# Kernel optimization log

Hardware: AMD Instinct MI355X
Metric: run time of the kernel (lower is better)

Reference implementation:

```python
import jax, jax.numpy as jnp
import numpy as np

B, L, HID = 32, 1, 3072
H, KV, D = 16, 8, 256
S = 2048
SCALE = D ** -0.5


def setup_inputs() -> dict:
    key = jax.random.key(0)
    ks = jax.random.split(key, 10)
    return {
        "hidden_states": jax.random.normal(ks[0], (B, L, HID), jnp.float32),
        "freqs_cos": jax.random.normal(ks[1], (B, L, D // 2), jnp.float32),
        "freqs_sin": jax.random.normal(ks[2], (B, L, D // 2), jnp.float32),
        "mask": jnp.zeros((B, 1, 1, S), jnp.float32),
        "cache_k": jax.random.normal(ks[3], (B, KV, S, D), jnp.float32),
        "cache_v": jax.random.normal(ks[4], (B, KV, S, D), jnp.float32),
        "wq": jax.random.normal(ks[5], (HID, H * D), jnp.float32) * 0.02,
        "wk": jax.random.normal(ks[6], (HID, KV * D), jnp.float32) * 0.02,
        "wv": jax.random.normal(ks[7], (HID, KV * D), jnp.float32) * 0.02,
        "wo": jax.random.normal(ks[8], (H * D, HID), jnp.float32) * 0.02,
        "pos": 2047,
    }


def _rope(x, cos, sin):
    # x: [B, L, nh, D]; cos/sin: [B, L, D/2]. Split-half complex rotation:
    # pairs are (x[..., i], x[..., i + D/2]), matching torch chunk+view_as_complex.
    half = x.shape[-1] // 2
    xr, xi = x[..., :half], x[..., half:]
    c = cos[:, :, None, :]
    s = sin[:, :, None, :]
    return jnp.concatenate([xr * c - xi * s, xr * s + xi * c], axis=-1)


def reference(hidden_states, freqs_cos, freqs_sin, mask, cache_k, cache_v,
              wq, wk, wv, wo, pos):
    G = H // KV  # queries per kv head
    xq = (hidden_states @ wq).reshape(B, L, H, D)
    xk = (hidden_states @ wk).reshape(B, L, KV, D)
    xv = (hidden_states @ wv).reshape(B, L, KV, D)

    xq = _rope(xq, freqs_cos, freqs_sin)
    xk = _rope(xk, freqs_cos, freqs_sin)

    # [B, heads, L, D]
    xq = xq.transpose(0, 2, 1, 3)
    xk = xk.transpose(0, 2, 1, 3)
    xv = xv.transpose(0, 2, 1, 3)

    # insert current step into the KV cache at static position `pos`
    cache_k = cache_k.at[:, :, pos:pos + L, :].set(xk)
    cache_v = cache_v.at[:, :, pos:pos + L, :].set(xv)

    # GQA attention over the full cache without materializing repeated KV
    q = xq.reshape(B, KV, G, L, D)
    scores = jnp.einsum('bkgqd,bksd->bkgqs', q, cache_k) * SCALE
    scores = scores + mask[:, :, None]  # [B,1,1,1,S] broadcast
    probs = jax.nn.softmax(scores, axis=-1)
    out = jnp.einsum('bkgqs,bksd->bkgqd', probs, cache_v)

    out = out.reshape(B, H, L, D).transpose(0, 2, 1, 3).reshape(B, L, H * D)
    return out @ wo
```

## Files before the change

kernel.cpp:

```cpp
#include <hip/hip_runtime.h>
#include <hip/hip_bf16.h>


#define SCALE_ 0.0625f

#define OFF_XQKV (8u*32u*8192u)
#define OFF_ATTN (OFF_XQKV + 32u*8192u)
#define OFF_PO   (OFF_ATTN + 32u*4096u)
#define OFF_ML   (1048576u)

__device__ inline void fma4(float4& a, float s, const float4& w) {
  a.x = fmaf(s, w.x, a.x); a.y = fmaf(s, w.y, a.y);
  a.z = fmaf(s, w.z, a.z); a.w = fmaf(s, w.w, a.w);
}
__device__ inline float dot4(const float4& a, const float4& b) {
  return a.x * b.x + a.y * b.y + a.z * b.z + a.w * b.w;
}

__global__ __launch_bounds__(512) void qkv_partial_kernel(
    const float* __restrict__ x, const float* __restrict__ wq,
    const float* __restrict__ wk, const float* __restrict__ wv,
    float* __restrict__ pqkv) {
  const int lane = threadIdx.x & 63;
  const int bg   = threadIdx.x >> 6;
  const int ctile = blockIdx.x & 31;
  const int kc    = blockIdx.x >> 5;
  const int n = ctile * 256 + lane * 4;

  const float* w; int stride, nn;
  if (n < 4096)      { w = wq; stride = 4096; nn = n; }
  else if (n < 6144) { w = wk; stride = 2048; nn = n - 4096; }
  else               { w = wv; stride = 2048; nn = n - 6144; }

  const float* wb = w + (size_t)(kc * 384) * stride + nn;
  const float* xb = x + (size_t)(bg * 4) * 3072 + kc * 384;

  float4 acc[4];
#pragma unroll
  for (int j = 0; j < 4; ++j) acc[j] = make_float4(0.f, 0.f, 0.f, 0.f);

  for (int k = 0; k < 384; k += 4) {
    float4 w0 = *(const float4*)(wb + (size_t)(k + 0) * stride);
    float4 w1 = *(const float4*)(wb + (size_t)(k + 1) * stride);
    float4 w2 = *(const float4*)(wb + (size_t)(k + 2) * stride);
    float4 w3 = *(const float4*)(wb + (size_t)(k + 3) * stride);
#pragma unroll
    for (int j = 0; j < 4; ++j) {
      float4 xv = *(const float4*)(xb + j * 3072 + k);
      fma4(acc[j], xv.x, w0);
      fma4(acc[j], xv.y, w1);
      fma4(acc[j], xv.z, w2);
      fma4(acc[j], xv.w, w3);
    }
  }
#pragma unroll
  for (int j = 0; j < 4; ++j) {
    *(float4*)(pqkv + ((size_t)kc * 32 + bg * 4 + j) * 8192 + n) = acc[j];
  }
}

__global__ __launch_bounds__(256) void reduce_rope_kernel(
    const float* __restrict__ pqkv, const float* __restrict__ fcos,
    const float* __restrict__ fsin, float* __restrict__ xqkv) {
  const int w = blockIdx.x * 256 + threadIdx.x;
  const int b = w / 5120;
  const int r = w - b * 5120;
  const float* pb = pqkv + (size_t)b * 8192;
  float* ob = xqkv + (size_t)b * 8192;

  if (r < 3072) {
    int n1, d;
    const bool isq = (r < 2048);
    if (isq) { int h = r >> 7; d = r & 127; n1 = h * 256 + d; }
    else     { int idx = r - 2048; int kvh = idx >> 7; d = idx & 127;
               n1 = 4096 + kvh * 256 + d; }
    const int n2 = n1 + 128;
    float xr = 0.f, xi = 0.f;
#pragma unroll
    for (int kc = 0; kc < 8; ++kc) {
      xr += pb[(size_t)kc * 262144 + n1];
      xi += pb[(size_t)kc * 262144 + n2];
    }
    const float c = fcos[b * 128 + d];
    const float s = fsin[b * 128 + d];
    float o1 = xr * c - xi * s;
    float o2 = xr * s + xi * c;
    if (isq) { o1 *= SCALE_; o2 *= SCALE_; }
    ob[n1] = o1;
    ob[n2] = o2;
  } else {
    const int nn = 6144 + (r - 3072);
    float v = 0.f;
#pragma unroll
    for (int kc = 0; kc < 8; ++kc) v += pb[(size_t)kc * 262144 + nn];
    ob[nn] = v;
  }
}

__global__ __launch_bounds__(256) void attn_chunk_kernel(
    const float* __restrict__ xqkv, const float* __restrict__ cache_k,
    const float* __restrict__ cache_v, const float* __restrict__ mask,
    const int* __restrict__ posp, float* __restrict__ opart,
    float* __restrict__ ml) {
  __shared__ float sc[2][256];
  __shared__ float accbuf[4][512];
  __shared__ float red0[4], red1[4];

  const int tid = threadIdx.x, lane = tid & 63, wv = tid >> 6;
  const int c  = blockIdx.x & 7;
  const int kv = (blockIdx.x >> 3) & 7;
  const int b  = blockIdx.x >> 6;
  const int pos = posp[0];
  const int s0 = c * 256;

  const float* xb = xqkv + (size_t)b * 8192;
  const float* knew = xb + 4096 + kv * 256;
  const float* vnew = xb + 6144 + kv * 256;
  const size_t base = ((size_t)b * 8 + kv) * 2048 * 256;
  const float* mrow = mask + (size_t)b * 2048;

  const int dbase = (lane & 31) * 8;
  const float4 qa0 = *(const float4*)(xb + (kv * 2 + 0) * 256 + dbase);
  const float4 qa1 = *(const float4*)(xb + (kv * 2 + 0) * 256 + dbase + 4);
  const float4 qb0 = *(const float4*)(xb + (kv * 2 + 1) * 256 + dbase);
  const float4 qb1 = *(const float4*)(xb + (kv * 2 + 1) * 256 + dbase + 4);

  for (int i = 0; i < 32; ++i) {
    const int sp = wv + 4 * i;
    const int sl = sp * 2 + (lane >> 5);
    const int s  = s0 + sl;
    const float* kr = (s == pos) ? knew : (cache_k + base + (size_t)s * 256);
    const float4 ka = *(const float4*)(kr + dbase);
    const float4 kb = *(const float4*)(kr + dbase + 4);
    float d0 = dot4(qa0, ka) + dot4(qa1, kb);
    float d1 = dot4(qb0, ka) + dot4(qb1, kb);
#pragma unroll
    for (int off = 16; off > 0; off >>= 1) {
      d0 += __shfl_xor(d0, off);
      d1 += __shfl_xor(d1, off);
    }
    if ((lane & 31) == 0) {
      const float mk = mrow[s];
      sc[0][sl] = d0 + mk;
      sc[1][sl] = d1 + mk;
    }
  }
  __syncthreads();

  const float v0 = sc[0][tid], v1 = sc[1][tid];
  float m0 = v0, m1 = v1;
#pragma unroll
  for (int off = 32; off > 0; off >>= 1) {
    m0 = fmaxf(m0, __shfl_xor(m0, off));
    m1 = fmaxf(m1, __shfl_xor(m1, off));
  }
  if (lane == 0) { red0[wv] = m0; red1[wv] = m1; }
  __syncthreads();
  m0 = fmaxf(fmaxf(red0[0], red0[1]), fmaxf(red0[2], red0[3]));
  m1 = fmaxf(fmaxf(red1[0], red1[1]), fmaxf(red1[2], red1[3]));
  const float e0 = __expf(v0 - m0), e1 = __expf(v1 - m1);
  sc[0][tid] = e0;
  sc[1][tid] = e1;
  float l0 = e0, l1 = e1;
#pragma unroll
  for (int off = 32; off > 0; off >>= 1) {
    l0 += __shfl_xor(l0, off);
    l1 += __shfl_xor(l1, off);
  }
  __syncthreads();
  if (lane == 0) { red0[wv] = l0; red1[wv] = l1; }
  __syncthreads();
  if (tid == 0) {
    l0 = red0[0] + red0[1] + red0[2] + red0[3];
    l1 = red1[0] + red1[1] + red1[2] + red1[3];
    float2* mlp = (float2*)ml;
    const int mlbase = (((b * 8 + kv) * 8) + c) * 2;
    mlp[mlbase + 0] = make_float2(m0, l0);
    mlp[mlbase + 1] = make_float2(m1, l1);
  }

  float4 a0 = make_float4(0.f, 0.f, 0.f, 0.f);
  float4 a1 = make_float4(0.f, 0.f, 0.f, 0.f);
  for (int i = 0; i < 64; ++i) {
    const int sl = wv + 4 * i;
    const int s = s0 + sl;
    const float* vr = (s == pos) ? vnew : (cache_v + base + (size_t)s * 256);
    const float4 v4 = *(const float4*)(vr + lane * 4);
    fma4(a0, sc[0][sl], v4);
    fma4(a1, sc[1][sl], v4);
  }
  *(float4*)(&accbuf[wv][lane * 4]) = a0;
  *(float4*)(&accbuf[wv][256 + lane * 4]) = a1;
  __syncthreads();
  const size_t obase = (size_t)((b * 8 + kv) * 8 + c) * 512;
  for (int t = tid; t < 512; t += 256) {
    opart[obase + t] = accbuf[0][t] + accbuf[1][t] + accbuf[2][t] + accbuf[3][t];
  }
}

__global__ __launch_bounds__(256) void attn_combine_kernel(
    const float* __restrict__ opart, const float* __restrict__ ml,
    float* __restrict__ attn_out) {
  const int idx = blockIdx.x * 256 + threadIdx.x;
  const int d = idx & 255;
  const int g = (idx >> 8) & 1;
  const int kvb = idx >> 9;
  const float2* mlp = (const float2*)ml;

  float2 mls[8];
  float M = -3.4e38f;
#pragma unroll
  for (int c = 0; c < 8; ++c) {
    mls[c] = mlp[(kvb * 8 + c) * 2 + g];
    M = fmaxf(M, mls[c].x);
  }
  float L = 0.f, O = 0.f;
#pragma unroll
  for (int c = 0; c < 8; ++c) {
    const float w = __expf(mls[c].x - M);
    L = fmaf(mls[c].y, w, L);
    O = fmaf(opart[(size_t)(kvb * 8 + c) * 512 + g * 256 + d], w, O);
  }
  const int b = kvb >> 3, kv = kvb & 7;
  attn_out[(size_t)b * 4096 + (kv * 2 + g) * 256 + d] = O / L;
}

__global__ __launch_bounds__(512) void oproj_partial_kernel(
    const float* __restrict__ attn, const float* __restrict__ wo,
    float* __restrict__ po) {
  const int lane = threadIdx.x & 63;
  const int bg   = threadIdx.x >> 6;
  const int ctile = blockIdx.x % 12;
  const int kc    = blockIdx.x / 12;
  const int n = ctile * 256 + lane * 4;

  const float* wb = wo + (size_t)(kc * 256) * 3072 + n;
  const float* xb = attn + (size_t)(bg * 4) * 4096 + kc * 256;

  float4 acc[4];
#pragma unroll
  for (int j = 0; j < 4; ++j) acc[j] = make_float4(0.f, 0.f, 0.f, 0.f);

  for (int k = 0; k < 256; k += 4) {
    float4 w0 = *(const float4*)(wb + (size_t)(k + 0) * 3072);
    float4 w1 = *(const float4*)(wb + (size_t)(k + 1) * 3072);
    float4 w2 = *(const float4*)(wb + (size_t)(k + 2) * 3072);
    float4 w3 = *(const float4*)(wb + (size_t)(k + 3) * 3072);
#pragma unroll
    for (int j = 0; j < 4; ++j) {
      float4 xv = *(const float4*)(xb + j * 4096 + k);
      fma4(acc[j], xv.x, w0);
      fma4(acc[j], xv.y, w1);
      fma4(acc[j], xv.z, w2);
      fma4(acc[j], xv.w, w3);
    }
  }
#pragma unroll
  for (int j = 0; j < 4; ++j) {
    *(float4*)(po + ((size_t)kc * 32 + bg * 4 + j) * 3072 + n) = acc[j];
  }
}

__global__ __launch_bounds__(256) void finalize_kernel(
    const float* __restrict__ po, float* __restrict__ out) {
  const int i = blockIdx.x * 256 + threadIdx.x;
  const float4* p = (const float4*)po;
  float4 acc = make_float4(0.f, 0.f, 0.f, 0.f);
#pragma unroll
  for (int kc = 0; kc < 16; ++kc) {
    const float4 v = p[(size_t)kc * 24576 + i];
    acc.x += v.x; acc.y += v.y; acc.z += v.z; acc.w += v.w;
  }
  ((float4*)out)[i] = acc;
}

extern "C" void kernel_launch(void* const* d_in, const int* in_sizes, int n_in,
                              void* d_out, int out_size, void* d_ws, size_t ws_size,
                              hipStream_t stream) {
  (void)in_sizes; (void)n_in; (void)out_size; (void)ws_size;
  const float* x    = (const float*)d_in[0];
  const float* fcos = (const float*)d_in[1];
  const float* fsin = (const float*)d_in[2];
  const float* mask = (const float*)d_in[3];
  const float* ck   = (const float*)d_in[4];
  const float* cv   = (const float*)d_in[5];
  const float* wq   = (const float*)d_in[6];
  const float* wk   = (const float*)d_in[7];
  const float* wv   = (const float*)d_in[8];
  const float* wo   = (const float*)d_in[9];
  const int*   pos  = (const int*)d_in[10];

  float* ws    = (float*)d_ws;
  float* pqkv  = ws;
  float* opart = ws;
  float* ml    = ws + OFF_ML;
  float* xqkv  = ws + OFF_XQKV;
  float* attn  = ws + OFF_ATTN;
  float* po    = ws + OFF_PO;
  float* out   = (float*)d_out;

  qkv_partial_kernel<<<256, 512, 0, stream>>>(x, wq, wk, wv, pqkv);
  reduce_rope_kernel<<<640, 256, 0, stream>>>(pqkv, fcos, fsin, xqkv);
  attn_chunk_kernel<<<2048, 256, 0, stream>>>(xqkv, ck, cv, mask, pos, opart, ml);
  attn_combine_kernel<<<512, 256, 0, stream>>>(opart, ml, attn);
  oproj_partial_kernel<<<192, 512, 0, stream>>>(attn, wo, po);
  finalize_kernel<<<96, 256, 0, stream>>>(po, out);
}
```

Before: 328.2 us.

## Fuse QK and PV passes into single-pass online softmax with prefetch

Rewrites the chunked attention kernel so each half-wave streams its own keys and values together and keeps a running max, sum and output (online softmax), instead of a score pass, a block softmax and then a separate value pass. Loads for the next row are issued one iteration ahead in software. This removes several block barriers and the shared score buffer and overlaps K/V loads with compute. In exchange it adds per-row exp rescaling, a larger accumulator buffer and an 8-way cross-stream merge, and K and V are now read with the same half-wave mapping.

```diff
diff --git a/kernel.cpp b/kernel.cpp
--- a/kernel.cpp
+++ b/kernel.cpp
@@ -15,6 +15,10 @@
 }
 __device__ inline float dot4(const float4& a, const float4& b) {
   return a.x * b.x + a.y * b.y + a.z * b.z + a.w * b.w;
+}
+__device__ inline void scale_fma4(float4& a, float sc, float p, const float4& v) {
+  a.x = fmaf(a.x, sc, p * v.x); a.y = fmaf(a.y, sc, p * v.y);
+  a.z = fmaf(a.z, sc, p * v.z); a.w = fmaf(a.w, sc, p * v.w);
 }
 
 __global__ __launch_bounds__(512) void qkv_partial_kernel(
@@ -102,99 +106,127 @@
     const float* __restrict__ cache_v, const float* __restrict__ mask,
     const int* __restrict__ posp, float* __restrict__ opart,
     float* __restrict__ ml) {
-  __shared__ float sc[2][256];
-  __shared__ float accbuf[4][512];
-  __shared__ float red0[4], red1[4];
+  __shared__ float accbuf[8][512];
+  __shared__ float mred[8][4];
 
   const int tid = threadIdx.x, lane = tid & 63, wv = tid >> 6;
+  const int sub = lane & 31;
+  const int stream = wv * 2 + (lane >> 5);
   const int c  = blockIdx.x & 7;
   const int kv = (blockIdx.x >> 3) & 7;
   const int b  = blockIdx.x >> 6;
   const int pos = posp[0];
   const int s0 = c * 256;
+  const int dbase = sub * 8;
 
   const float* xb = xqkv + (size_t)b * 8192;
   const float* knew = xb + 4096 + kv * 256;
   const float* vnew = xb + 6144 + kv * 256;
   const size_t base = ((size_t)b * 8 + kv) * 2048 * 256;
+  const float* kbase = cache_k + base;
+  const float* vbase = cache_v + base;
   const float* mrow = mask + (size_t)b * 2048;
 
-  const int dbase = (lane & 31) * 8;
   const float4 qa0 = *(const float4*)(xb + (kv * 2 + 0) * 256 + dbase);
   const float4 qa1 = *(const float4*)(xb + (kv * 2 + 0) * 256 + dbase + 4);
   const float4 qb0 = *(const float4*)(xb + (kv * 2 + 1) * 256 + dbase);
   const float4 qb1 = *(const float4*)(xb + (kv * 2 + 1) * 256 + dbase + 4);
 
-  for (int i = 0; i < 32; ++i) {
-    const int sp = wv + 4 * i;
-    const int sl = sp * 2 + (lane >> 5);
-    const int s  = s0 + sl;
-    const float* kr = (s == pos) ? knew : (cache_k + base + (size_t)s * 256);
-    const float4 ka = *(const float4*)(kr + dbase);
-    const float4 kb = *(const float4*)(kr + dbase + 4);
-    float d0 = dot4(qa0, ka) + dot4(qa1, kb);
-    float d1 = dot4(qb0, ka) + dot4(qb1, kb);
-#pragma unroll
-    for (int off = 16; off > 0; off >>= 1) {
-      d0 += __shfl_xor(d0, off);
-      d1 += __shfl_xor(d1, off);
-    }
-    if ((lane & 31) == 0) {
-      const float mk = mrow[s];
-      sc[0][sl] = d0 + mk;
-      sc[1][sl] = d1 + mk;
-    }
+  float m0 = -3.4e38f, l0 = 0.f, m1 = -3.4e38f, l1 = 0.f;
+  float4 a00 = make_float4(0.f, 0.f, 0.f, 0.f);
+  float4 a01 = make_float4(0.f, 0.f, 0.f, 0.f);
+  float4 a10 = make_float4(0.f, 0.f, 0.f, 0.f);
+  float4 a11 = make_float4(0.f, 0.f, 0.f, 0.f);
+
+  {
+    const int s = s0 + stream;
+    const float* kr = (s == pos) ? knew : (kbase + (size_t)s * 256);
+    const float* vr = (s == pos) ? vnew : (vbase + (size_t)s * 256);
+    float4 ka = *(const float4*)(kr + dbase);
+    float4 kb = *(const float4*)(kr + dbase + 4);
+    float4 va = *(const float4*)(vr + dbase);
+    float4 vb = *(const float4*)(vr + dbase + 4);
+    float mk = mrow[s];
+
+    for (int i = 0; i < 32; ++i) {
+      const float4 cka = ka, ckb = kb, cva = va, cvb = vb;
+      const float cmk = mk;
+      if (i < 31) {
+        const int s2 = s0 + stream + 8 * (i + 1);
+        const float* kr2 = (s2 == pos) ? knew : (kbase + (size_t)s2 * 256);
+        const float* vr2 = (s2 == pos) ? vnew : (vbase + (size_t)s2 * 256);
+        ka = *(const float4*)(kr2 + dbase);
+        kb = *(const float4*)(kr2 + dbase + 4);
+        va = *(const float4*)(vr2 + dbase);
+        vb = *(const float4*)(vr2 + dbase + 4);
+        mk = mrow[s2];
+      }
+      float d0 = dot4(qa0, cka) + dot4(qa1, ckb);
+      float d1 = dot4(qb0, cka) + dot4(qb1, ckb);
+#pragma unroll
+      for (int off = 16; off > 0; off >>= 1) {
+        d0 += __shfl_xor(d0, off);
+        d1 += __shfl_xor(d1, off);
+      }
+      d0 += cmk; d1 += cmk;
+      const float nm0 = fmaxf(m0, d0);
+      const float al0 = __expf(m0 - nm0);
+      const float p0  = __expf(d0 - nm0);
+      m0 = nm0; l0 = fmaf(l0, al0, p0);
+      scale_fma4(a00, al0, p0, cva);
+      scale_fma4(a01, al0, p0, cvb);
+      const float nm1 = fmaxf(m1, d1);
+      const float al1 = __expf(m1 - nm1);
+      const float p1  = __expf(d1 - nm1);
+      m1 = nm1; l1 = fmaf(l1, al1, p1);
+      scale_fma4(a10, al1, p1, cva);
+      scale_fma4(a11, al1, p1, cvb);
+    }
+  }
+
+  if (sub == 0) {
+    mred[stream][0] = m0; mred[stream][1] = l0;
+    mred[stream][2] = m1; mred[stream][3] = l1;
   }
   __syncthreads();
-
-  const float v0 = sc[0][tid], v1 = sc[1][tid];
-  float m0 = v0, m1 = v1;
-#pragma unroll
-  for (int off = 32; off > 0; off >>= 1) {
-    m0 = fmaxf(m0, __shfl_xor(m0, off));
-    m1 = fmaxf(m1, __shfl_xor(m1, off));
-  }
-  if (lane == 0) { red0[wv] = m0; red1[wv] = m1; }
+  float M0 = -3.4e38f, M1 = -3.4e38f;
+#pragma unroll
+  for (int t = 0; t < 8; ++t) {
+    M0 = fmaxf(M0, mred[t][0]);
+    M1 = fmaxf(M1, mred[t][2]);
+  }
+  const float sc0 = __expf(m0 - M0);
+  const float sc1 = __expf(m1 - M1);
+  float* ab = &accbuf[stream][0];
+  ab[dbase + 0] = a00.x * sc0; ab[dbase + 1] = a00.y * sc0;
+  ab[dbase + 2] = a00.z * sc0; ab[dbase + 3] = a00.w * sc0;
+  ab[dbase + 4] = a01.x * sc0; ab[dbase + 5] = a01.y * sc0;
+  ab[dbase + 6] = a01.z * sc0; ab[dbase + 7] = a01.w * sc0;
+  ab[256 + dbase + 0] = a10.x * sc1; ab[256 + dbase + 1] = a10.y * sc1;
+  ab[256 + dbase + 2] = a10.z * sc1; ab[256 + dbase + 3] = a10.w * sc1;
+  ab[256 + dbase + 4] = a11.x * sc1; ab[256 + dbase + 5] = a11.y * sc1;
+  ab[256 + dbase + 6] = a11.z * sc1; ab[256 + dbase + 7] = a11.w * sc1;
   __syncthreads();
-  m0 = fmaxf(fmaxf(red0[0], red0[1]), fmaxf(red0[2], red0[3]));
-  m1 = fmaxf(fmaxf(red1[0], red1[1]), fmaxf(red1[2], red1[3]));
-  const float e0 = __expf(v0 - m0), e1 = __expf(v1 - m1);
-  sc[0][tid] = e0;
-  sc[1][tid] = e1;
-  float l0 = e0, l1 = e1;
-#pragma unroll
-  for (int off = 32; off > 0; off >>= 1) {
-    l0 += __shfl_xor(l0, off);
-    l1 += __shfl_xor(l1, off);
-  }
-  __syncthreads();
-  if (lane == 0) { red0[wv] = l0; red1[wv] = l1; }
-  __syncthreads();
+
   if (tid == 0) {
-    l0 = red0[0] + red0[1] + red0[2] + red0[3];
-    l1 = red1[0] + red1[1] + red1[2] + red1[3];
+    float L0 = 0.f, L1 = 0.f;
+#pragma unroll
+    for (int t = 0; t < 8; ++t) {
+      L0 = fmaf(mred[t][1], __expf(mred[t][0] - M0), L0);
+      L1 = fmaf(mred[t][3], __expf(mred[t][2] - M1), L1);
+    }
     float2* mlp = (float2*)ml;
     const int mlbase = (((b * 8 + kv) * 8) + c) * 2;
-    mlp[mlbase + 0] = make_float2(m0, l0);
-    mlp[mlbase + 1] = make_float2(m1, l1);
-  }
-
-  float4 a0 = make_float4(0.f, 0.f, 0.f, 0.f);
-  float4 a1 = make_float4(0.f, 0.f, 0.f, 0.f);
-  for (int i = 0; i < 64; ++i) {
-    const int sl = wv + 4 * i;
-    const int s = s0 + sl;
-    const float* vr = (s == pos) ? vnew : (cache_v + base + (size_t)s * 256);
-    const float4 v4 = *(const float4*)(vr + lane * 4);
-    fma4(a0, sc[0][sl], v4);
-    fma4(a1, sc[1][sl], v4);
-  }
-  *(float4*)(&accbuf[wv][lane * 4]) = a0;
-  *(float4*)(&accbuf[wv][256 + lane * 4]) = a1;
-  __syncthreads();
+    mlp[mlbase + 0] = make_float2(M0, L0);
+    mlp[mlbase + 1] = make_float2(M1, L1);
+  }
+
   const size_t obase = (size_t)((b * 8 + kv) * 8 + c) * 512;
   for (int t = tid; t < 512; t += 256) {
-    opart[obase + t] = accbuf[0][t] + accbuf[1][t] + accbuf[2][t] + accbuf[3][t];
+    float sum = 0.f;
+#pragma unroll
+    for (int st = 0; st < 8; ++st) sum += accbuf[st][t];
+    opart[obase + t] = sum;
   }
 }
 
```

New measurement: 329.7 us. Within noise of the previous version (+0.5%).
